# Kernel optimization log

Measured on AMD Instinct MI355X. Metric: run time of the kernel, lower is better.

Reference implementation:

```python
import jax, jax.numpy as jnp
import numpy as np

B, S, H, R, DEPTH = 64, 32, 1024, 256, 9  # batch, seq, hidden, GRU hidden (h//reduction), tree depth


def _gru(x, h, W_ih, W_hh, b_ih, b_hh):
    # PyTorch nn.GRUCell math
    gi = x @ W_ih.T + b_ih
    gh = h @ W_hh.T + b_hh
    i_r, i_z, i_n = jnp.split(gi, 3, axis=-1)
    h_r, h_z, h_n = jnp.split(gh, 3, axis=-1)
    r = jax.nn.sigmoid(i_r + h_r)
    z = jax.nn.sigmoid(i_z + h_z)
    n = jnp.tanh(i_n + r * h_n)
    return (1.0 - z) * n + z * h


def _forward(x, W_hidden, b_hidden, W_hb, b_hb, W_branch, b_branch, W_ih, W_hh, b_ih, b_hh, tree_depth):
    selu = jax.nn.selu
    # root: discretize(selu(hidden(selu(x)))).mean over sequence; discretize=identity (discretize kw None)
    xc = selu(selu(x) @ W_hidden.T + b_hidden).mean(axis=1)[:, None, :]  # [B,1,H]
    hc = jnp.zeros((x.shape[0], 1, W_hh.shape[1]), x.dtype)              # [B,1,R]
    depth = jnp.zeros((x.shape[0], 1, 1), x.dtype)
    for _ in range(tree_depth):  # level-synchronous expansion of the recursive generate()
        hc = _gru(xc, hc, W_ih, W_hh, b_ih, b_hh)
        xh = jnp.concatenate([xc, hc], axis=-1)                          # [B,N,H+R]
        hb = jax.nn.sigmoid(xh @ W_hb.T + b_hb)                          # [B,N,1]
        depth = depth + hb
        lr = selu(xh @ W_branch.T + b_branch)                            # [B,N,2H]
        l, r = jnp.split(lr, 2, axis=-1)
        l = xc - selu(l @ W_hidden.T + b_hidden)                          # residual left child
        r = xc - selu(r @ W_hidden.T + b_hidden)                          # residual right child
        Bn, N, Hd = xc.shape
        xc = jnp.stack([l, r], axis=2).reshape(Bn, 2 * N, Hd)
        hc = jnp.repeat(hc, 2, axis=1)
        depth = jnp.repeat(depth, 2, axis=1)
    # leaf nodes: final controller step; terminal = x (no V head), depth += has_branches
    hc = _gru(xc, hc, W_ih, W_hh, b_ih, b_hh)
    hb = jax.nn.sigmoid(jnp.concatenate([xc, hc], axis=-1) @ W_hb.T + b_hb)
    depth = depth + hb
    return jnp.concatenate([xc, depth], axis=-1)  # [B, 2**D, H+1]: leaf terminals + leaf depths


def setup_inputs() -> dict:
    key = jax.random.key(0)
    ks = jax.random.split(key, 6)
    def w(k, o, i):
        return (jax.random.normal(k, (o, i), jnp.float32) / np.sqrt(i)).astype(jnp.float32)
    return {
        'x': jax.random.normal(ks[0], (B, S, H), jnp.float32),
        'W_hidden': w(ks[1], H, H), 'b_hidden': jnp.zeros((H,), jnp.float32),
        'W_hb': w(ks[2], 1, H + R), 'b_hb': jnp.zeros((1,), jnp.float32),
        'W_branch': w(ks[3], 2 * H, H + R), 'b_branch': jnp.zeros((2 * H,), jnp.float32),
        'W_ih': w(ks[4], 3 * R, H), 'W_hh': w(ks[5], 3 * R, R),
        'b_ih': jnp.zeros((3 * R,), jnp.float32), 'b_hh': jnp.zeros((3 * R,), jnp.float32),
        'tree_depth': DEPTH,
    }


def reference(x, W_hidden, b_hidden, W_hb, b_hb, W_branch, b_branch, W_ih, W_hh, b_ih, b_hh, tree_depth):
    return _forward(x, W_hidden, b_hidden, W_hb, b_hb, W_branch, b_branch, W_ih, W_hh, b_ih, b_hh, tree_depth)
```

## Files before the change

### kernel.cpp

```cpp
#include <hip/hip_runtime.h>
#include <hip/hip_bf16.h>
#include <cstdint>
#include <cstddef>


#define SELU_L 1.0507009873554805f
#define SELU_A 1.6732632423543772f

__device__ __forceinline__ float selu_f(float x) {
    return x > 0.f ? SELU_L * x : (SELU_L * SELU_A) * (__expf(x) - 1.f);
}
__device__ __forceinline__ float sigmoid_f(float x) {
    return 1.f / (1.f + __expf(-x));
}

typedef __attribute__((ext_vector_type(8))) short s16x8;
typedef __attribute__((ext_vector_type(4))) float f32x4;

__device__ __forceinline__ void gld16(const void* g, void* l) {
    __builtin_amdgcn_global_load_lds(
        (const __attribute__((address_space(1))) uint32_t*)g,
        (__attribute__((address_space(3))) uint32_t*)l, 16, 0, 0);
}

enum { AM_PLAIN = 0, AM_CONCAT = 2 };
enum { EP_NONE = 0, EP_SELU32 = 1, EP_BRANCH = 2, EP_RESID = 3 };

template <int AMODE, int EPI>
__device__ __forceinline__ void gemm_body(
    int bm, int bn, int M, int K,
    const __hip_bfloat16* __restrict__ A, int lda,
    const __hip_bfloat16* __restrict__ A2,
    const __hip_bfloat16* __restrict__ W,
    const float* __restrict__ bias,
    void* __restrict__ Cv, int ldc,
    const __hip_bfloat16* __restrict__ P,
    float* __restrict__ C32, int ldc32,
    short* As, short* Bs)
{
    const int tid  = threadIdx.x;
    const int wave = tid >> 6;
    const int lane = tid & 63;

    const short* gA[4]; const short* gA2p[4]; const short* gB[4];
    short* dA[4]; short* dB[4];
#pragma unroll
    for (int r = 0; r < 4; ++r) {
        const int s   = r * 256 + wave * 64 + lane;
        const int row = s >> 3;
        const int pc  = s & 7;
        const int j   = (pc - (row >> 1)) & 7;
        const int ga  = min(bm + row, M - 1);
        if (AMODE == AM_CONCAT) {
            gA[r]   = (const short*)A  + (size_t)ga * 1024 + j * 8;
            gA2p[r] = (const short*)A2 + (size_t)ga * 256  + j * 8;
        } else {
            gA[r]   = (const short*)A + (size_t)ga * lda + j * 8;
            gA2p[r] = nullptr;
        }
        gB[r] = (const short*)W + (size_t)(bn + row) * K + j * 8;
        dA[r] = &As[(size_t)(r * 256 + wave * 64) * 8];
        dB[r] = &Bs[(size_t)(r * 256 + wave * 64) * 8];
    }

    const int wm = (wave >> 1) * 64, wn = (wave & 1) * 64;
    const int l16 = lane & 15, q4 = lane >> 4;
    int aoff[4], boff[4];
#pragma unroll
    for (int i = 0; i < 4; ++i) {
        int ra = wm + i * 16 + l16;
        aoff[i] = ra * 64 + (((q4 + (ra >> 1)) & 7) << 3);
        int rb = wn + i * 16 + l16;
        boff[i] = rb * 64 + (((q4 + (rb >> 1)) & 7) << 3);
    }

    f32x4 acc[4][4] = {};

    for (int k0 = 0; k0 < K; k0 += 64) {
#pragma unroll
        for (int r = 0; r < 4; ++r) {
            const short* ap;
            if (AMODE == AM_CONCAT)
                ap = (k0 < 1024) ? gA[r] + k0 : gA2p[r] + (k0 - 1024);
            else
                ap = gA[r] + k0;
            gld16(ap, dA[r]);
            gld16(gB[r] + k0, dB[r]);
        }
        __syncthreads();

#pragma unroll
        for (int h = 0; h < 2; ++h) {
            const int hx = h << 5;
            s16x8 af[4], bf[4];
#pragma unroll
            for (int i = 0; i < 4; ++i) af[i] = *(const s16x8*)&As[aoff[i] ^ hx];
#pragma unroll
            for (int i = 0; i < 4; ++i) bf[i] = *(const s16x8*)&Bs[boff[i] ^ hx];
#pragma unroll
            for (int mi = 0; mi < 4; ++mi)
#pragma unroll
                for (int ni = 0; ni < 4; ++ni)
                    acc[mi][ni] = __builtin_amdgcn_mfma_f32_16x16x32_bf16(
                        af[mi], bf[ni], acc[mi][ni], 0, 0, 0);
        }
        __syncthreads();
    }

    const int crow0 = bm + wm + q4 * 4;
    const int ccol0 = bn + wn + l16;
#pragma unroll
    for (int mi = 0; mi < 4; ++mi) {
#pragma unroll
        for (int r = 0; r < 4; ++r) {
            const int row = crow0 + mi * 16 + r;
            if (row >= M) continue;
#pragma unroll
            for (int ni = 0; ni < 4; ++ni) {
                const int col = ccol0 + ni * 16;
                float v = acc[mi][ni][r] + bias[col];
                if (EPI == EP_NONE) {
                    ((float*)Cv)[(size_t)row * ldc + col] = v;
                } else if (EPI == EP_SELU32) {
                    ((float*)Cv)[(size_t)row * ldc + col] = selu_f(v);
                } else if (EPI == EP_BRANCH) {
                    const int c = col >> 10, jj = col & 1023;
                    ((__hip_bfloat16*)Cv)[(size_t)(2 * row + c) * 1024 + jj] =
                        __float2bfloat16(selu_f(v));
                } else {
                    const float pv = __bfloat162float(P[(size_t)(row >> 1) * 1024 + col]);
                    const float o = pv - selu_f(v);
                    ((__hip_bfloat16*)Cv)[(size_t)row * 1024 + col] = __float2bfloat16(o);
                    if (C32) C32[(size_t)row * ldc32 + col] = o;
                }
            }
        }
    }
}

template <int AMODE, int EPI>
__global__ __launch_bounds__(256) void mgemm(
    int M, int N, int K,
    const __hip_bfloat16* __restrict__ A, int lda,
    const __hip_bfloat16* __restrict__ A2,
    const __hip_bfloat16* __restrict__ W,
    const float* __restrict__ bias,
    void* __restrict__ Cv, int ldc,
    const __hip_bfloat16* __restrict__ P,
    float* __restrict__ C32, int ldc32)
{
    __shared__ short As[8192];
    __shared__ short Bs[8192];
    int bxi = blockIdx.x, byi = blockIdx.y;
    {
        const int ncol = gridDim.x, nrow = gridDim.y;
        if ((nrow & 7) == 0) {
            const int lin = byi * ncol + bxi;
            const int xcd = lin & 7;
            const int t = lin >> 3;
            const int rows_per = nrow >> 3;
            bxi = t % ncol;
            byi = xcd * rows_per + t / ncol;
        }
    }
    gemm_body<AMODE, EPI>(byi * 128, bxi * 128, M, K, A, lda, A2, W, bias,
                          Cv, ldc, P, C32, ldc32, As, Bs);
}

struct GPair {
    int M0, K0; const __hip_bfloat16* A0; int lda0;
    const __hip_bfloat16* W0; const float* b0; float* C0; int ldc0;
    int M1, K1; const __hip_bfloat16* A1; int lda1;
    const __hip_bfloat16* W1; const float* b1; float* C1; int ldc1;
};
__global__ __launch_bounds__(256) void mgemm_pair(GPair g)
{
    __shared__ short As[8192];
    __shared__ short Bs[8192];
    int bxi = blockIdx.x, byi = blockIdx.y;
    if (blockIdx.z == 0) {
        const int ncol = gridDim.x, nrow = gridDim.y;
        if ((nrow & 7) == 0) {
            const int lin = byi * ncol + bxi;
            const int xcd = lin & 7;
            const int t = lin >> 3;
            const int rows_per = nrow >> 3;
            bxi = t % ncol;
            byi = xcd * rows_per + t / ncol;
        }
        gemm_body<AM_PLAIN, EP_NONE>(byi * 128, bxi * 128, g.M0, g.K0,
                                     g.A0, g.lda0, nullptr, g.W0, g.b0,
                                     g.C0, g.ldc0, nullptr, nullptr, 0, As, Bs);
    } else {
        if (byi * 128 >= g.M1) return;
        gemm_body<AM_PLAIN, EP_NONE>(byi * 128, bxi * 128, g.M1, g.K1,
                                     g.A1, g.lda1, nullptr, g.W1, g.b1,
                                     g.C1, g.ldc1, nullptr, nullptr, 0, As, Bs);
    }
}

template <int AMODE, int EPI>
__device__ __forceinline__ void gemm256_body(
    int bm, int bn, int M, int K,
    const __hip_bfloat16* __restrict__ A, int lda,
    const __hip_bfloat16* __restrict__ A2,
    const __hip_bfloat16* __restrict__ W,
    const float* __restrict__ bias,
    void* __restrict__ Cv, int ldc,
    const __hip_bfloat16* __restrict__ P,
    float* __restrict__ C32, int ldc32,
    short* As, short* Bs)
{
    const int tid  = threadIdx.x;
    const int wave = tid >> 6;
    const int lane = tid & 63;
    const int wm = (wave >> 2) * 128;
    const int wn = (wave & 3) * 64;
    const int l16 = lane & 15, q4 = lane >> 4;

    const short* gA[2]; const short* gA2p[2]; const short* gB[2];
    int dOf[2];
#pragma unroll
    for (int r = 0; r < 2; ++r) {
        const int s   = r * 512 + tid;
        const int row = s >> 2;
        const int pc  = s & 3;
        const int j   = (pc - (row >> 1)) & 3;
        const int ga  = min(bm + row, M - 1);
        if (AMODE == AM_CONCAT) {
            gA[r]   = (const short*)A  + (size_t)ga * 1024 + j * 8;
            gA2p[r] = (const short*)A2 + (size_t)ga * 256  + j * 8;
        } else {
            gA[r]   = (const short*)A + (size_t)ga * lda + j * 8;
            gA2p[r] = nullptr;
        }
        gB[r]  = (const short*)W + (size_t)(bn + row) * K + j * 8;
        dOf[r] = (r * 512 + wave * 64) * 8;
    }

    int aof[2][4], bof[4];
#pragma unroll
    for (int mh = 0; mh < 2; ++mh)
#pragma unroll
        for (int i = 0; i < 4; ++i) {
            const int ra = wm + mh * 64 + i * 16 + l16;
            aof[mh][i] = ra * 32 + (((q4 + (ra >> 1)) & 3) << 3);
        }
#pragma unroll
    for (int n = 0; n < 4; ++n) {
        const int rb = wn + n * 16 + l16;
        bof[n] = rb * 32 + (((q4 + (rb >> 1)) & 3) << 3);
    }

    f32x4 acc[8][4] = {};
    const int NT = K >> 5;

#pragma unroll
    for (int r = 0; r < 2; ++r) gld16(gA[r], &As[dOf[r]]);
#pragma unroll
    for (int r = 0; r < 2; ++r) gld16(gB[r], &Bs[dOf[r]]);
    asm volatile("s_waitcnt vmcnt(0)" ::: "memory");
    __builtin_amdgcn_s_barrier();

    for (int t = 0; t < NT; ++t) {
        const int cur = (t & 1) << 13;
        const int nxt = 8192 - cur;
        const int k1  = (t + 1) << 5;

        if (t + 1 < NT) {
#pragma unroll
            for (int r = 0; r < 2; ++r) {
                const short* ap;
                if (AMODE == AM_CONCAT)
                    ap = (k1 < 1024) ? gA[r] + k1 : gA2p[r] + (k1 - 1024);
                else
                    ap = gA[r] + k1;
                gld16(ap, &As[nxt + dOf[r]]);
            }
#pragma unroll
            for (int r = 0; r < 2; ++r) gld16(gB[r] + k1, &Bs[nxt + dOf[r]]);
        }
        s16x8 af[4], bf[4];
#pragma unroll
        for (int i = 0; i < 4; ++i) af[i] = *(const s16x8*)&As[cur + aof[0][i]];
#pragma unroll
        for (int n = 0; n < 4; ++n) bf[n] = *(const s16x8*)&Bs[cur + bof[n]];
        __builtin_amdgcn_s_barrier();
        __builtin_amdgcn_s_setprio(1);
#pragma unroll
        for (int mi = 0; mi < 4; ++mi)
#pragma unroll
            for (int n = 0; n < 4; ++n)
                acc[mi][n] = __builtin_amdgcn_mfma_f32_16x16x32_bf16(
                    af[mi], bf[n], acc[mi][n], 0, 0, 0);
        __builtin_amdgcn_s_setprio(0);
        __builtin_amdgcn_s_barrier();

#pragma unroll
        for (int i = 0; i < 4; ++i) af[i] = *(const s16x8*)&As[cur + aof[1][i]];
        __builtin_amdgcn_s_barrier();
        __builtin_amdgcn_s_setprio(1);
#pragma unroll
        for (int mi = 0; mi < 4; ++mi)
#pragma unroll
            for (int n = 0; n < 4; ++n)
                acc[4 + mi][n] = __builtin_amdgcn_mfma_f32_16x16x32_bf16(
                    af[mi], bf[n], acc[4 + mi][n], 0, 0, 0);
        __builtin_amdgcn_s_setprio(0);
        asm volatile("s_waitcnt vmcnt(0)" ::: "memory");
        __builtin_amdgcn_s_barrier();
    }

    const int crow0 = bm + wm + q4 * 4;
    const int ccol0 = bn + wn + l16;
#pragma unroll
    for (int m8 = 0; m8 < 8; ++m8) {
#pragma unroll
        for (int r = 0; r < 4; ++r) {
            const int row = crow0 + m8 * 16 + r;
            if (row >= M) continue;
#pragma unroll
            for (int n4 = 0; n4 < 4; ++n4) {
                const int col = ccol0 + n4 * 16;
                float v = acc[m8][n4][r] + bias[col];
                if (EPI == EP_NONE) {
                    ((float*)Cv)[(size_t)row * ldc + col] = v;
                } else if (EPI == EP_SELU32) {
                    ((float*)Cv)[(size_t)row * ldc + col] = selu_f(v);
                } else if (EPI == EP_BRANCH) {
                    const int c = col >> 10, jj = col & 1023;
                    ((__hip_bfloat16*)Cv)[(size_t)(2 * row + c) * 1024 + jj] =
                        __float2bfloat16(selu_f(v));
                } else {
                    const float pv = __bfloat162float(P[(size_t)(row >> 1) * 1024 + col]);
                    const float o = pv - selu_f(v);
                    ((__hip_bfloat16*)Cv)[(size_t)row * 1024 + col] = __float2bfloat16(o);
                    if (C32) C32[(size_t)row * ldc32 + col] = o;
                }
            }
        }
    }
}

template <int AMODE, int EPI>
__global__ __launch_bounds__(512) void mgemm256(
    int M, int N, int K,
    const __hip_bfloat16* __restrict__ A, int lda,
    const __hip_bfloat16* __restrict__ A2,
    const __hip_bfloat16* __restrict__ W,
    const float* __restrict__ bias,
    void* __restrict__ Cv, int ldc,
    const __hip_bfloat16* __restrict__ P,
    float* __restrict__ C32, int ldc32)
{
    __shared__ short As[16384];
    __shared__ short Bs[16384];
    int bxi = blockIdx.x, byi = blockIdx.y;
    {
        const int ncol = gridDim.x, nrow = gridDim.y;
        if ((nrow & 7) == 0) {
            const int lin = byi * ncol + bxi;
            const int xcd = lin & 7;
            const int t = lin >> 3;
            const int rows_per = nrow >> 3;
            bxi = t % ncol;
            byi = xcd * rows_per + t / ncol;
        }
    }
    gemm256_body<AMODE, EPI>(byi * 256, bxi * 256, M, K, A, lda, A2, W, bias,
                             Cv, ldc, P, C32, ldc32, As, Bs);
}

__global__ void cvt4_k(const float* __restrict__ s0, __hip_bfloat16* __restrict__ d0, int n0,
                       const float* __restrict__ s1, __hip_bfloat16* __restrict__ d1, int n1,
                       const float* __restrict__ s2, __hip_bfloat16* __restrict__ d2, int n2,
                       const float* __restrict__ s3, __hip_bfloat16* __restrict__ d3, int n3)
{
    int i = blockIdx.x * 256 + threadIdx.x;
    if (i < n0) { d0[i] = __float2bfloat16(s0[i]); return; }
    i -= n0;
    if (i < n1) { d1[i] = __float2bfloat16(s1[i]); return; }
    i -= n1;
    if (i < n2) { d2[i] = __float2bfloat16(s2[i]); return; }
    i -= n2;
    if (i < n3) { d3[i] = __float2bfloat16(s3[i]); }
}

__global__ void selu_cvt_k(const float* __restrict__ in, __hip_bfloat16* __restrict__ out, int n)
{
    int i = blockIdx.x * 256 + threadIdx.x;
    if (i < n) out[i] = __float2bfloat16(selu_f(in[i]));
}

__global__ void mean_kernel(const float* __restrict__ T, __hip_bfloat16* __restrict__ xc)
{
    const int idx = blockIdx.x * 256 + threadIdx.x;
    const int b = idx >> 10, h = idx & 1023;
    const float* p = T + (size_t)b * 32 * 1024 + h;
    float s = 0.f;
#pragma unroll
    for (int si = 0; si < 32; ++si) s += p[si * 1024];
    xc[idx] = __float2bfloat16(s * (1.f / 32.f));
}

__global__ __launch_bounds__(256) void gateshb_kernel(
    const float* __restrict__ gi,
    const float* __restrict__ gh,
    const float* __restrict__ b_hh,
    const __hip_bfloat16* __restrict__ hold,
    __hip_bfloat16* __restrict__ hnew,
    const __hip_bfloat16* __restrict__ xc,
    const float* __restrict__ W_hb,
    const float* __restrict__ b_hb,
    const float* __restrict__ depth_old,
    float* __restrict__ depth_out, int dstride,
    int first)
{
    const int m = blockIdx.x;
    const int j = threadIdx.x;
    __shared__ float red[4];

    const float* gim = gi + (size_t)m * 768;
    const float ir = gim[j], iz = gim[256 + j], in_ = gim[512 + j];
    float hr, hz, hn, h0;
    if (first) {
        hr = b_hh[j]; hz = b_hh[256 + j]; hn = b_hh[512 + j]; h0 = 0.f;
    } else {
        const float* ghm = gh + (size_t)(m >> 1) * 768;
        hr = ghm[j]; hz = ghm[256 + j]; hn = ghm[512 + j];
        h0 = __bfloat162float(hold[(size_t)(m >> 1) * 256 + j]);
    }
    const float r = sigmoid_f(ir + hr);
    const float z = sigmoid_f(iz + hz);
    const float n = tanhf(in_ + r * hn);
    const float hv = (1.f - z) * n + z * h0;
    hnew[(size_t)m * 256 + j] = __float2bfloat16(hv);

    const __hip_bfloat16* xr = xc + (size_t)m * 1024;
    float s = hv * W_hb[1024 + j];
#pragma unroll
    for (int kk = 0; kk < 4; ++kk) {
        const int k = j + kk * 256;
        s += __bfloat162float(xr[k]) * W_hb[k];
    }
#pragma unroll
    for (int off = 32; off; off >>= 1) s += __shfl_down(s, off);
    if ((j & 63) == 0) red[j >> 6] = s;
    __syncthreads();
    if (j == 0) {
        const float tot = red[0] + red[1] + red[2] + red[3];
        const float hb = sigmoid_f(tot + b_hb[0]);
        const float d0 = first ? 0.f : depth_old[m >> 1];
        depth_out[(size_t)m * dstride] = d0 + hb;
    }
}

extern "C" void kernel_launch(void* const* d_in, const int* in_sizes, int n_in,
                              void* d_out, int out_size, void* d_ws, size_t ws_size,
                              hipStream_t stream)
{
    const float* x        = (const float*)d_in[0];
    const float* W_hidden = (const float*)d_in[1];
    const float* b_hidden = (const float*)d_in[2];
    const float* W_hb     = (const float*)d_in[3];
    const float* b_hb     = (const float*)d_in[4];
    const float* W_branch = (const float*)d_in[5];
    const float* b_branch = (const float*)d_in[6];
    const float* W_ih     = (const float*)d_in[7];
    const float* W_hh     = (const float*)d_in[8];
    const float* b_ih     = (const float*)d_in[9];
    const float* b_hh     = (const float*)d_in[10];

    char* ws = (char*)d_ws;
    size_t off = 0;
    auto alloc = [&](size_t bytes) {
        void* p = ws + off;
        off += (bytes + 255) & ~(size_t)255;
        return p;
    };
    __hip_bfloat16* Whb  = (__hip_bfloat16*)alloc(1024 * 1024 * 2);
    __hip_bfloat16* Wbb  = (__hip_bfloat16*)alloc(2048 * 1280 * 2);
    __hip_bfloat16* Wib  = (__hip_bfloat16*)alloc(768 * 1024 * 2);
    __hip_bfloat16* Whh  = (__hip_bfloat16*)alloc(768 * 256 * 2);
    __hip_bfloat16* Xs   = (__hip_bfloat16*)alloc((size_t)2048 * 1024 * 2);
    float*          GI   = (float*)alloc((size_t)32768 * 768 * 4);
    __hip_bfloat16* U    = (__hip_bfloat16*)alloc((size_t)32768 * 1024 * 2);
    __hip_bfloat16* XC0  = (__hip_bfloat16*)alloc((size_t)32768 * 1024 * 2);
    __hip_bfloat16* XC1  = (__hip_bfloat16*)alloc((size_t)32768 * 1024 * 2);
    __hip_bfloat16* HC0  = (__hip_bfloat16*)alloc((size_t)32768 * 256 * 2);
    __hip_bfloat16* HC1  = (__hip_bfloat16*)alloc((size_t)32768 * 256 * 2);
    float*          D0   = (float*)alloc(32768 * 4);
    float*          D1   = (float*)alloc(32768 * 4);
    float*          GH   = (float*)U;

    float* out = (float*)d_out;

    {
        const int n0 = 1024 * 1024, n1 = 2048 * 1280, n2 = 768 * 1024, n3 = 768 * 256;
        cvt4_k<<<(n0 + n1 + n2 + n3 + 255) / 256, 256, 0, stream>>>(
            W_hidden, Whb, n0, W_branch, Wbb, n1, W_ih, Wib, n2, W_hh, Whh, n3);
    }
    selu_cvt_k<<<(2048 * 1024 + 255) / 256, 256, 0, stream>>>(x, Xs, 2048 * 1024);

    mgemm<AM_PLAIN, EP_SELU32><<<dim3(1024 / 128, 2048 / 128), 256, 0, stream>>>(
        2048, 1024, 1024, Xs, 1024, nullptr, Whb, b_hidden, GI, 1024, nullptr, nullptr, 0);
    mean_kernel<<<(64 * 1024) / 256, 256, 0, stream>>>(GI, XC0);

    __hip_bfloat16* xc_cur = XC0; __hip_bfloat16* xc_next = XC1;
    __hip_bfloat16* hc_prev = nullptr; __hip_bfloat16* hc_new = HC0;
    float* d_prev = nullptr; float* d_next = D0;

    for (int d = 0; d < 9; ++d) {
        const int M = 64 << d;
        GPair g;
        g.M0 = M;     g.K0 = 1024; g.A0 = xc_cur;  g.lda0 = 1024;
        g.W0 = Wib;   g.b0 = b_ih; g.C0 = GI;      g.ldc0 = 768;
        g.M1 = M / 2; g.K1 = 256;  g.A1 = hc_prev; g.lda1 = 256;
        g.W1 = Whh;   g.b1 = b_hh; g.C1 = GH;      g.ldc1 = 768;
        mgemm_pair<<<dim3(768 / 128, (M + 127) / 128, d > 0 ? 2 : 1), 256, 0, stream>>>(g);

        gateshb_kernel<<<M, 256, 0, stream>>>(
            GI, (const float*)GH, b_hh, hc_prev, hc_new,
            xc_cur, W_hb, b_hb, d_prev, d_next, 1, d == 0 ? 1 : 0);

        if (d >= 7) {
            mgemm256<AM_CONCAT, EP_BRANCH><<<dim3(2048 / 256, M / 256), 512, 0, stream>>>(
                M, 2048, 1280, xc_cur, 1024, hc_new, Wbb, b_branch, U, 1024,
                nullptr, nullptr, 0);
            mgemm256<AM_PLAIN, EP_RESID><<<dim3(1024 / 256, (2 * M) / 256), 512, 0, stream>>>(
                2 * M, 1024, 1024, U, 1024, nullptr, Whb, b_hidden, xc_next, 1024,
                xc_cur, d == 8 ? out : nullptr, 1025);
        } else {
            mgemm<AM_CONCAT, EP_BRANCH><<<dim3(2048 / 128, (M + 127) / 128), 256, 0, stream>>>(
                M, 2048, 1280, xc_cur, 1024, hc_new, Wbb, b_branch, U, 1024,
                nullptr, nullptr, 0);
            mgemm<AM_PLAIN, EP_RESID><<<dim3(1024 / 128, (2 * M) / 128), 256, 0, stream>>>(
                2 * M, 1024, 1024, U, 1024, nullptr, Whb, b_hidden, xc_next, 1024,
                xc_cur, d == 8 ? out : nullptr, 1025);
        }

        __hip_bfloat16* t = xc_cur; xc_cur = xc_next; xc_next = t;
        hc_prev = hc_new; hc_new = (hc_new == HC0) ? HC1 : HC0;
        d_prev = d_next;  d_next = (d_next == D0) ? D1 : D0;
    }

    {
        const int M = 32768;
        mgemm256<AM_PLAIN, EP_NONE><<<dim3(768 / 256, M / 256), 512, 0, stream>>>(
            M, 768, 1024, xc_cur, 1024, nullptr, Wib, b_ih, GI, 768,
            nullptr, nullptr, 0);
        mgemm<AM_PLAIN, EP_NONE><<<dim3(768 / 128, (M / 2) / 128), 256, 0, stream>>>(
            M / 2, 768, 256, hc_prev, 256, nullptr, Whh, b_hh, (void*)GH, 768,
            nullptr, nullptr, 0);
        gateshb_kernel<<<M, 256, 0, stream>>>(
            GI, (const float*)GH, b_hh, hc_prev, hc_new,
            xc_cur, W_hb, b_hb, d_prev, out + 1024, 1025, 0);
    }
}
```

Measured before the change: 1.596 ms.

## Deepen 256-tile GEMM pipeline to four LDS stages with three tiles in flight

```diff
diff --git a/kernel.cpp b/kernel.cpp
--- a/kernel.cpp
+++ b/kernel.cpp
@@ -238,14 +238,12 @@
         dOf[r] = (r * 512 + wave * 64) * 8;
     }
 
-    int aof[2][4], bof[4];
-#pragma unroll
-    for (int mh = 0; mh < 2; ++mh)
-#pragma unroll
-        for (int i = 0; i < 4; ++i) {
-            const int ra = wm + mh * 64 + i * 16 + l16;
-            aof[mh][i] = ra * 32 + (((q4 + (ra >> 1)) & 3) << 3);
-        }
+    int aof[8], bof[4];
+#pragma unroll
+    for (int m = 0; m < 8; ++m) {
+        const int ra = wm + m * 16 + l16;
+        aof[m] = ra * 32 + (((q4 + (ra >> 1)) & 3) << 3);
+    }
 #pragma unroll
     for (int n = 0; n < 4; ++n) {
         const int rb = wn + n * 16 + l16;
@@ -255,61 +253,50 @@
     f32x4 acc[8][4] = {};
     const int NT = K >> 5;
 
-#pragma unroll
-    for (int r = 0; r < 2; ++r) gld16(gA[r], &As[dOf[r]]);
-#pragma unroll
-    for (int r = 0; r < 2; ++r) gld16(gB[r], &Bs[dOf[r]]);
-    asm volatile("s_waitcnt vmcnt(0)" ::: "memory");
-    __builtin_amdgcn_s_barrier();
-
-    for (int t = 0; t < NT; ++t) {
-        const int cur = (t & 1) << 13;
-        const int nxt = 8192 - cur;
-        const int k1  = (t + 1) << 5;
-
-        if (t + 1 < NT) {
-#pragma unroll
-            for (int r = 0; r < 2; ++r) {
-                const short* ap;
-                if (AMODE == AM_CONCAT)
-                    ap = (k1 < 1024) ? gA[r] + k1 : gA2p[r] + (k1 - 1024);
-                else
-                    ap = gA[r] + k1;
-                gld16(ap, &As[nxt + dOf[r]]);
-            }
-#pragma unroll
-            for (int r = 0; r < 2; ++r) gld16(gB[r] + k1, &Bs[nxt + dOf[r]]);
-        }
-        s16x8 af[4], bf[4];
-#pragma unroll
-        for (int i = 0; i < 4; ++i) af[i] = *(const s16x8*)&As[cur + aof[0][i]];
-#pragma unroll
-        for (int n = 0; n < 4; ++n) bf[n] = *(const s16x8*)&Bs[cur + bof[n]];
-        __builtin_amdgcn_s_barrier();
-        __builtin_amdgcn_s_setprio(1);
-#pragma unroll
-        for (int mi = 0; mi < 4; ++mi)
-#pragma unroll
-            for (int n = 0; n < 4; ++n)
-                acc[mi][n] = __builtin_amdgcn_mfma_f32_16x16x32_bf16(
-                    af[mi], bf[n], acc[mi][n], 0, 0, 0);
-        __builtin_amdgcn_s_setprio(0);
-        __builtin_amdgcn_s_barrier();
-
-#pragma unroll
-        for (int i = 0; i < 4; ++i) af[i] = *(const s16x8*)&As[cur + aof[1][i]];
-        __builtin_amdgcn_s_barrier();
-        __builtin_amdgcn_s_setprio(1);
-#pragma unroll
-        for (int mi = 0; mi < 4; ++mi)
-#pragma unroll
-            for (int n = 0; n < 4; ++n)
-                acc[4 + mi][n] = __builtin_amdgcn_mfma_f32_16x16x32_bf16(
-                    af[mi], bf[n], acc[4 + mi][n], 0, 0, 0);
-        __builtin_amdgcn_s_setprio(0);
-        asm volatile("s_waitcnt vmcnt(0)" ::: "memory");
-        __builtin_amdgcn_s_barrier();
-    }
+    auto stage = [&](int t) {
+        const int k0 = t << 5;
+        const int sb = (t & 3) << 13;
+#pragma unroll
+        for (int r = 0; r < 2; ++r) {
+            const short* ap;
+            if (AMODE == AM_CONCAT)
+                ap = (k0 < 1024) ? gA[r] + k0 : gA2p[r] + (k0 - 1024);
+            else
+                ap = gA[r] + k0;
+            gld16(ap, &As[sb + dOf[r]]);
+        }
+#pragma unroll
+        for (int r = 0; r < 2; ++r) gld16(gB[r] + k0, &Bs[sb + dOf[r]]);
+    };
+
+    stage(0); stage(1); stage(2);
+
+#define STEP256(t_, DOISS_, VMS_) do {                                        \
+        asm volatile("s_waitcnt vmcnt(" VMS_ ")" ::: "memory");               \
+        __builtin_amdgcn_s_barrier();                                         \
+        asm volatile("" ::: "memory");      \
+        const int cur_ = ((t_) & 3) << 13;                                    \
+        s16x8 af_[8], bf_[4];                                                 \
+        _Pragma("unroll")                                                     \
+        for (int m = 0; m < 8; ++m) af_[m] = *(const s16x8*)&As[cur_ + aof[m]]; \
+        _Pragma("unroll")                                                     \
+        for (int n = 0; n < 4; ++n) bf_[n] = *(const s16x8*)&Bs[cur_ + bof[n]]; \
+        if (DOISS_) stage((t_) + 3);                                          \
+        __builtin_amdgcn_s_setprio(1);                                        \
+        _Pragma("unroll")                                                     \
+        for (int m = 0; m < 8; ++m)                                           \
+            _Pragma("unroll")                                                 \
+            for (int n = 0; n < 4; ++n)                                       \
+                acc[m][n] = __builtin_amdgcn_mfma_f32_16x16x32_bf16(          \
+                    af_[m], bf_[n], acc[m][n], 0, 0, 0);                      \
+        __builtin_amdgcn_s_setprio(0);                                        \
+    } while (0)
+
+    for (int t = 0; t < NT - 3; ++t) STEP256(t, 1, "8");
+    STEP256(NT - 3, 0, "8");
+    STEP256(NT - 2, 0, "4");
+    STEP256(NT - 1, 0, "0");
+#undef STEP256
 
     const int crow0 = bm + wm + q4 * 4;
     const int ccol0 = bn + wn + l16;
@@ -353,8 +340,8 @@
     const __hip_bfloat16* __restrict__ P,
     float* __restrict__ C32, int ldc32)
 {
-    __shared__ short As[16384];
-    __shared__ short Bs[16384];
+    __shared__ short As[32768];
+    __shared__ short Bs[32768];
     int bxi = blockIdx.x, byi = blockIdx.y;
     {
         const int ncol = gridDim.x, nrow = gridDim.y;
```

After: 1.469 ms (median of 2 runs). -8.0%, faster.
